# Performance work log

Hardware: AMD Instinct MI355X
Metric: run time of the kernel (lower is better)

The kernel has to match this reference:

```python
import jax, jax.numpy as jnp
import numpy as np

B, T, HID = 1, 2048, 2048
H = 16            # num_heads == num_key_value_heads
D = HID // H      # head_dim == feature_dim == 128
EPS = 1e-5


def _layer_norm(x, eps=1e-5):
    mu = jnp.mean(x, axis=-1, keepdims=True)
    var = jnp.mean((x - mu) ** 2, axis=-1, keepdims=True)
    return (x - mu) * jax.lax.rsqrt(var + eps)


def _feature_map(x, gamma, beta):
    # ReBased feature map, flatten=False (parallel mode): affine then LayerNorm
    return _layer_norm(x * gamma + beta)


def setup_inputs() -> dict:
    key = jax.random.key(0)
    ks = jax.random.split(key, 8)
    s = HID ** -0.5
    return {
        "hidden_states": jax.random.normal(ks[0], (B, T, HID), jnp.float32),
        "Wq": jax.random.normal(ks[1], (HID, HID), jnp.float32) * s,
        "Wk": jax.random.normal(ks[2], (HID, HID), jnp.float32) * s,
        "Wv": jax.random.normal(ks[3], (HID, HID), jnp.float32) * s,
        "Wo": jax.random.normal(ks[4], (HID, HID), jnp.float32) * s,
        "gamma": 1.0 + 0.1 * jax.random.normal(ks[5], (D,), jnp.float32),
        "beta": 0.1 * jax.random.normal(ks[6], (D,), jnp.float32),
    }


def reference(hidden_states, Wq, Wk, Wv, Wo, gamma, beta):
    b, t, _ = hidden_states.shape
    # projections (nn.Linear: x @ W.T), split into heads: [b, t, h, d]
    q = (hidden_states @ Wq.T).reshape(b, t, H, D)
    k = (hidden_states @ Wk.T).reshape(b, t, H, D)
    v = (hidden_states @ Wv.T).reshape(b, t, H, D)
    # ReBased feature map (no quadratic flatten in parallel mode)
    q = _feature_map(q, gamma, beta)
    k = _feature_map(k, gamma, beta)
    # parallel_rebased: scale q, quadratic score, causal mask, normalize
    q = q * (D ** -0.5)
    attn = jnp.einsum('bqhd,bkhd->bhqk', q, k) ** 2  # (q.k)^2
    mask = jnp.tril(jnp.ones((t, t), dtype=bool))
    attn = jnp.where(mask, attn, 0.0)
    o = jnp.einsum('bhqk,bkhd->bqhd', attn, v)       # [b, t, h, d]
    z = jnp.sum(attn, axis=-1)                       # [b, h, t]
    o = o / (jnp.swapaxes(z, 1, 2)[..., None] + EPS)
    o = o.reshape(b, t, H * D)
    return o @ Wo.T
```

## Files before the change

### kernel.cpp

```cpp
#include <hip/hip_runtime.h>
#include <hip/hip_bf16.h>
#include <stdint.h>

typedef __bf16 bf16;
typedef __bf16 v8bf __attribute__((ext_vector_type(8)));
typedef float  v4f  __attribute__((ext_vector_type(4)));

#define TSEQ   2048
#define HIDDIM 2048
#define NHEAD  16
#define HDIM   128

__device__ __forceinline__ void async16(void* lds, const void* g)
{
    __builtin_amdgcn_global_load_lds(
        (__attribute__((address_space(1))) void*)(uintptr_t)g,
        (__attribute__((address_space(3))) void*)(unsigned int)(uintptr_t)lds,
        16, 0, 0);
}

__global__ __launch_bounds__(256) void conv5(const float* __restrict__ s0, bf16* __restrict__ d0,
                                             const float* __restrict__ s1, bf16* __restrict__ d1,
                                             const float* __restrict__ s2, bf16* __restrict__ d2,
                                             const float* __restrict__ s3, bf16* __restrict__ d3,
                                             const float* __restrict__ s4, bf16* __restrict__ d4)
{
    const float* src; bf16* dst;
    switch (blockIdx.y) {
        case 0: src = s0; dst = d0; break;
        case 1: src = s1; dst = d1; break;
        case 2: src = s2; dst = d2; break;
        case 3: src = s3; dst = d3; break;
        default: src = s4; dst = d4; break;
    }
    const size_t i = ((size_t)blockIdx.x * 256 + threadIdx.x) * 8;
    const float4 a = *(const float4*)(src + i);
    const float4 b = *(const float4*)(src + i + 4);
    v8bf o;
    o[0] = (bf16)a.x; o[1] = (bf16)a.y; o[2] = (bf16)a.z; o[3] = (bf16)a.w;
    o[4] = (bf16)b.x; o[5] = (bf16)b.y; o[6] = (bf16)b.z; o[7] = (bf16)b.w;
    *(v8bf*)(dst + i) = o;
}

template <typename CT>
__device__ __forceinline__ void gemm_body(const bf16* __restrict__ A,
                                          const bf16* __restrict__ B,
                                          CT* __restrict__ C,
                                          int m0, int n0, int K, int ldc)
{
    __shared__ __attribute__((aligned(16))) bf16 sA[128*32];
    __shared__ __attribute__((aligned(16))) bf16 sB[128*32];
    const int tid  = threadIdx.x;
    const int lane = tid & 63;
    const int w    = tid >> 6;
    const int wm   = w >> 1, wn = w & 1;
    const int quad = lane >> 4, lr = lane & 15;
    const int srow = lane >> 2;
    const int scol = (lane & 3) * 8;

    const bf16* gA0 = A + (size_t)(m0 + w*32 + srow) * K + scol;
    const bf16* gB0 = B + (size_t)(n0 + w*32 + srow) * K + scol;
    bf16* lA0 = &sA[w*1024];
    bf16* lB0 = &sB[w*1024];

    v4f acc[4][4] = {};

    for (int kt = 0; kt < K; kt += 32) {
        __syncthreads();
        async16(lA0,       gA0 + kt);
        async16(lA0 + 512, gA0 + (size_t)16*K + kt);
        async16(lB0,       gB0 + kt);
        async16(lB0 + 512, gB0 + (size_t)16*K + kt);
        __syncthreads();
        v8bf a[4], b[4];
#pragma unroll
        for (int i = 0; i < 4; ++i)
            a[i] = *(const v8bf*)&sA[(wm*64 + i*16 + lr)*32 + quad*8];
#pragma unroll
        for (int j = 0; j < 4; ++j)
            b[j] = *(const v8bf*)&sB[(wn*64 + j*16 + lr)*32 + quad*8];
#pragma unroll
        for (int i = 0; i < 4; ++i)
#pragma unroll
            for (int j = 0; j < 4; ++j)
                acc[i][j] = __builtin_amdgcn_mfma_f32_16x16x32_bf16(a[i], b[j], acc[i][j], 0, 0, 0);
    }

#pragma unroll
    for (int i = 0; i < 4; ++i) {
        const int row_b = m0 + wm*64 + i*16 + quad*4;
#pragma unroll
        for (int j = 0; j < 4; ++j) {
            const int col = n0 + wn*64 + j*16 + lr;
#pragma unroll
            for (int r = 0; r < 4; ++r)
                C[(size_t)(row_b + r)*ldc + col] = (CT)acc[i][j][r];
        }
    }
}

__global__ __launch_bounds__(256) void gemm_qkv(const bf16* __restrict__ A,
    const bf16* __restrict__ Wq, const bf16* __restrict__ Wk, const bf16* __restrict__ Wv,
    bf16* __restrict__ qb, bf16* __restrict__ kb, bf16* __restrict__ vb)
{
    const int which = blockIdx.x >> 4;
    const int n0 = (blockIdx.x & 15) * 128;
    const int m0 = blockIdx.y * 128;
    const bf16* B = (which == 0) ? Wq : (which == 1) ? Wk : Wv;
    bf16* C = (which == 0) ? qb : (which == 1) ? kb : vb;
    gemm_body<bf16>(A, B, C, m0, n0, HIDDIM, HIDDIM);
}

__global__ __launch_bounds__(256) void gemm_out(const bf16* __restrict__ A,
    const bf16* __restrict__ B, float* __restrict__ C)
{
    __shared__ __attribute__((aligned(16))) bf16 sA[128*32];
    __shared__ __attribute__((aligned(16))) bf16 sB[64*32];
    const int m0 = blockIdx.y * 128, n0 = blockIdx.x * 64;
    const int K = HIDDIM, ldc = HIDDIM;
    const int tid  = threadIdx.x;
    const int lane = tid & 63;
    const int w    = tid >> 6;
    const int wm   = w >> 1, wn = w & 1;
    const int quad = lane >> 4, lr = lane & 15;
    const int srow = lane >> 2;
    const int scol = (lane & 3) * 8;

    const bf16* gA0 = A + (size_t)(m0 + w*32 + srow) * K + scol;
    const bf16* gB0 = B + (size_t)(n0 + w*16 + srow) * K + scol;
    bf16* lA0 = &sA[w*1024];
    bf16* lB0 = &sB[w*512];

    v4f acc[4][2] = {};

    for (int kt = 0; kt < K; kt += 32) {
        __syncthreads();
        async16(lA0,       gA0 + kt);
        async16(lA0 + 512, gA0 + (size_t)16*K + kt);
        async16(lB0,       gB0 + kt);
        __syncthreads();
        v8bf a[4], b[2];
#pragma unroll
        for (int i = 0; i < 4; ++i)
            a[i] = *(const v8bf*)&sA[(wm*64 + i*16 + lr)*32 + quad*8];
#pragma unroll
        for (int j = 0; j < 2; ++j)
            b[j] = *(const v8bf*)&sB[(wn*32 + j*16 + lr)*32 + quad*8];
#pragma unroll
        for (int i = 0; i < 4; ++i)
#pragma unroll
            for (int j = 0; j < 2; ++j)
                acc[i][j] = __builtin_amdgcn_mfma_f32_16x16x32_bf16(a[i], b[j], acc[i][j], 0, 0, 0);
    }

#pragma unroll
    for (int i = 0; i < 4; ++i) {
        const int row_b = m0 + wm*64 + i*16 + quad*4;
#pragma unroll
        for (int j = 0; j < 2; ++j) {
            const int col = n0 + wn*32 + j*16 + lr;
#pragma unroll
            for (int r = 0; r < 4; ++r)
                C[(size_t)(row_b + r)*ldc + col] = acc[i][j][r];
        }
    }
}

__global__ __launch_bounds__(256) void fmap(bf16* __restrict__ qb, bf16* __restrict__ kb,
                                            const float* __restrict__ gamma,
                                            const float* __restrict__ beta)
{
    const int rid  = blockIdx.x * 4 + (threadIdx.x >> 6);
    const int lane = threadIdx.x & 63;
    bf16* base = (rid < TSEQ*NHEAD) ? (qb + (size_t)rid * HDIM)
                                    : (kb + (size_t)(rid - TSEQ*NHEAD) * HDIM);
    const float scale = (rid < TSEQ*NHEAD) ? 0.08838834764831845f : 1.0f;

    const bf16 x0b = base[lane*2], x1b = base[lane*2+1];
    const float g0 = gamma[lane*2], g1 = gamma[lane*2+1];
    const float b0 = beta[lane*2],  b1 = beta[lane*2+1];
    float x0 = (float)x0b*g0 + b0;
    float x1 = (float)x1b*g1 + b1;
    float s  = x0 + x1;
    float sq = x0*x0 + x1*x1;
#pragma unroll
    for (int off = 1; off < 64; off <<= 1) { s += __shfl_xor(s, off); sq += __shfl_xor(sq, off); }
    const float mu   = s * (1.0f/128.0f);
    float var        = sq * (1.0f/128.0f) - mu*mu;
    var = fmaxf(var, 0.0f);
    const float rstd = rsqrtf(var + 1e-5f);
    base[lane*2]   = (bf16)((x0 - mu) * rstd * scale);
    base[lane*2+1] = (bf16)((x1 - mu) * rstd * scale);
}

__global__ __launch_bounds__(256) void transpose2048(const bf16* __restrict__ src,
                                                     bf16* __restrict__ dst)
{
    __shared__ __attribute__((aligned(16))) bf16 tile[64][72];
    const int t0 = blockIdx.y * 64, c0 = blockIdx.x * 64;
    const int tid = threadIdx.x;
    const int r = tid >> 3;
    const int c = (tid & 7) * 8;
#pragma unroll
    for (int p = 0; p < 2; ++p) {
        const int rr = r + p*32;
        *(v8bf*)&tile[rr][c] = *(const v8bf*)(src + (size_t)(t0+rr)*HIDDIM + c0 + c);
    }
    __syncthreads();
#pragma unroll
    for (int p = 0; p < 2; ++p) {
        const int orow = r + p*32;
        v8bf o;
#pragma unroll
        for (int i = 0; i < 8; ++i) o[i] = tile[c + i][orow];
        *(v8bf*)(dst + (size_t)(c0+orow)*HIDDIM + t0 + c) = o;
    }
}

__global__ __launch_bounds__(256) void attn(const bf16* __restrict__ qb,
                                            const bf16* __restrict__ kb,
                                            const bf16* __restrict__ vt,
                                            bf16* __restrict__ ob)
{
    __shared__ __attribute__((aligned(16))) bf16 sK[64*136];
    __shared__ __attribute__((aligned(16))) bf16 sV[128*72];
    __shared__ __attribute__((aligned(16))) bf16 sS[64*72];
    const int h    = blockIdx.y;
    const int tile = 31 - blockIdx.x;
    const int tid  = threadIdx.x, lane = tid & 63, w = tid >> 6;
    const int quad = lane >> 4, lr = lane & 15;

    v8bf qa[4];
    {
        const bf16* q0 = qb + (size_t)(tile*64 + w*16 + lr)*HIDDIM + h*HDIM + quad*8;
#pragma unroll
        for (int ks = 0; ks < 4; ++ks)
            qa[ks] = *(const v8bf*)(q0 + ks*32);
    }

    const int rK = tid >> 4, cK = (tid & 15) * 8;
    const int rV = tid >> 3, cV = (tid & 7) * 8;

    v8bf curK[4], curV[4], nxtK[4], nxtV[4];
#pragma unroll
    for (int p = 0; p < 4; ++p) {
        curK[p] = *(const v8bf*)(kb + (size_t)(rK + p*16)*HIDDIM + h*HDIM + cK);
        curV[p] = *(const v8bf*)(vt + (size_t)(h*HDIM + rV + p*32)*HIDDIM + cV);
    }

    v4f  o[8] = {};
    float z[4] = {};
    const int nch = tile + 1;

    for (int ch = 0; ch < nch; ++ch) {
        const int s0 = ch * 64;
        const bool diag = (ch == tile);
        __syncthreads();
#pragma unroll
        for (int p = 0; p < 4; ++p)
            *(v8bf*)&sK[(rK + p*16)*136 + cK] = curK[p];
#pragma unroll
        for (int p = 0; p < 4; ++p)
            *(v8bf*)&sV[(rV + p*32)*72 + cV] = curV[p];
        if (ch + 1 < nch) {
            const int s1 = s0 + 64;
#pragma unroll
            for (int p = 0; p < 4; ++p) {
                nxtK[p] = *(const v8bf*)(kb + (size_t)(s1 + rK + p*16)*HIDDIM + h*HDIM + cK);
                nxtV[p] = *(const v8bf*)(vt + (size_t)(h*HDIM + rV + p*32)*HIDDIM + s1 + cV);
            }
        }
        __syncthreads();

        v8bf kbf[4][4];
#pragma unroll
        for (int nj = 0; nj < 4; ++nj)
#pragma unroll
            for (int ks = 0; ks < 4; ++ks)
                kbf[nj][ks] = *(const v8bf*)&sK[(nj*16 + lr)*136 + ks*32 + quad*8];
        const int row_l = w*16 + quad*4;
        const int qg    = tile*64 + row_l;
#pragma unroll
        for (int nj = 0; nj < 4; ++nj) {
            v4f s4 = {0.f, 0.f, 0.f, 0.f};
#pragma unroll
            for (int ks = 0; ks < 4; ++ks)
                s4 = __builtin_amdgcn_mfma_f32_16x16x32_bf16(qa[ks], kbf[nj][ks], s4, 0, 0, 0);
            const int col = nj*16 + lr;
            const int sg  = s0 + col;
#pragma unroll
            for (int r = 0; r < 4; ++r) {
                float val = s4[r] * s4[r];
                if (diag && (sg > qg + r)) val = 0.0f;
                const bf16 vb16 = (bf16)val;
                z[r] += (float)vb16;
                sS[(row_l + r)*72 + col] = vb16;
            }
        }

#pragma unroll
        for (int ks = 0; ks < 2; ++ks) {
            const v8bf sa = *(const v8bf*)&sS[(w*16 + lr)*72 + ks*32 + quad*8];
#pragma unroll
            for (int nd = 0; nd < 8; ++nd) {
                const v8bf vbf = *(const v8bf*)&sV[(nd*16 + lr)*72 + ks*32 + quad*8];
                o[nd] = __builtin_amdgcn_mfma_f32_16x16x32_bf16(sa, vbf, o[nd], 0, 0, 0);
            }
        }

        if (ch + 1 < nch) {
#pragma unroll
            for (int p = 0; p < 4; ++p) { curK[p] = nxtK[p]; curV[p] = nxtV[p]; }
        }
    }

#pragma unroll
    for (int r = 0; r < 4; ++r) {
        float zz = z[r];
        zz += __shfl_xor(zz, 1); zz += __shfl_xor(zz, 2);
        zz += __shfl_xor(zz, 4); zz += __shfl_xor(zz, 8);
        z[r] = zz + 1e-5f;
    }

    {
        const int row_l = w*16 + quad*4;
        const size_t rbase = (size_t)(tile*64 + row_l)*HIDDIM + h*HDIM;
#pragma unroll
        for (int nd = 0; nd < 8; ++nd) {
            const int col = nd*16 + lr;
#pragma unroll
            for (int r = 0; r < 4; ++r)
                ob[rbase + (size_t)r*HIDDIM + col] = (bf16)(o[nd][r] / z[r]);
        }
    }
}

extern "C" void kernel_launch(void* const* d_in, const int* in_sizes, int n_in,
                              void* d_out, int out_size, void* d_ws, size_t ws_size,
                              hipStream_t stream)
{
    const float* hs    = (const float*)d_in[0];
    const float* Wq    = (const float*)d_in[1];
    const float* Wk    = (const float*)d_in[2];
    const float* Wv    = (const float*)d_in[3];
    const float* Wo    = (const float*)d_in[4];
    const float* gamma = (const float*)d_in[5];
    const float* beta  = (const float*)d_in[6];
    float* outp = (float*)d_out;

    const size_t MAT = (size_t)TSEQ * HIDDIM;

    bf16* ws   = (bf16*)d_ws;
    bf16* hs_b = ws + 0*MAT;
    bf16* vt   = hs_b;
    bf16* Wv_b = ws + 1*MAT;
    bf16* Wo_b = ws + 2*MAT;
    bf16* qb   = ws + 3*MAT;
    bf16* kb   = ws + 4*MAT;
    bf16* vb   = ws + 5*MAT;
    bf16* ob   = vb;
    bf16* Wq_b = (bf16*)d_out;
    bf16* Wk_b = (bf16*)d_out + MAT;

    conv5<<<dim3(2048, 5), 256, 0, stream>>>(hs, hs_b, Wq, Wq_b, Wk, Wk_b, Wv, Wv_b, Wo, Wo_b);
    gemm_qkv<<<dim3(48, 16), 256, 0, stream>>>(hs_b, Wq_b, Wk_b, Wv_b, qb, kb, vb);
    fmap<<<dim3(2*TSEQ*NHEAD/4), 256, 0, stream>>>(qb, kb, gamma, beta);
    transpose2048<<<dim3(32, 32), 256, 0, stream>>>(vb, vt);
    attn<<<dim3(32, 16), 256, 0, stream>>>(qb, kb, vt, ob);
    gemm_out<<<dim3(32, 16), 256, 0, stream>>>(ob, Wo_b, outp);
}
```

Measured before the change: 301.4 us.

## Fuse feature-map LayerNorm and V transpose into QKV GEMM epilogue

```diff
diff --git a/kernel.cpp b/kernel.cpp
--- a/kernel.cpp
+++ b/kernel.cpp
@@ -42,14 +42,21 @@
     *(v8bf*)(dst + i) = o;
 }
 
-template <typename CT>
-__device__ __forceinline__ void gemm_body(const bf16* __restrict__ A,
-                                          const bf16* __restrict__ B,
-                                          CT* __restrict__ C,
-                                          int m0, int n0, int K, int ldc)
+__global__ __launch_bounds__(256) void gemm_qkv(const bf16* __restrict__ A,
+    const bf16* __restrict__ Wq, const bf16* __restrict__ Wk, const bf16* __restrict__ Wv,
+    const float* __restrict__ gamma, const float* __restrict__ beta,
+    bf16* __restrict__ qb, bf16* __restrict__ kb, bf16* __restrict__ vt)
 {
     __shared__ __attribute__((aligned(16))) bf16 sA[128*32];
     __shared__ __attribute__((aligned(16))) bf16 sB[128*32];
+    __shared__ __attribute__((aligned(16))) bf16 sEpi[128*136];
+
+    const int which = blockIdx.x >> 4;
+    const int n0 = (blockIdx.x & 15) * 128;
+    const int m0 = blockIdx.y * 128;
+    const bf16* B = (which == 0) ? Wq : (which == 1) ? Wk : Wv;
+    const int K = HIDDIM;
+
     const int tid  = threadIdx.x;
     const int lane = tid & 63;
     const int w    = tid >> 6;
@@ -86,29 +93,83 @@
                 acc[i][j] = __builtin_amdgcn_mfma_f32_16x16x32_bf16(a[i], b[j], acc[i][j], 0, 0, 0);
     }
 
-#pragma unroll
-    for (int i = 0; i < 4; ++i) {
-        const int row_b = m0 + wm*64 + i*16 + quad*4;
+    if (which < 2) {
+        bf16* C = (which == 0) ? qb : kb;
+        const float scale = (which == 0) ? 0.08838834764831845f : 1.0f;
+        float g[4], bt[4];
 #pragma unroll
         for (int j = 0; j < 4; ++j) {
-            const int col = n0 + wn*64 + j*16 + lr;
-#pragma unroll
-            for (int r = 0; r < 4; ++r)
-                C[(size_t)(row_b + r)*ldc + col] = (CT)acc[i][j][r];
-        }
-    }
-}
-
-__global__ __launch_bounds__(256) void gemm_qkv(const bf16* __restrict__ A,
-    const bf16* __restrict__ Wq, const bf16* __restrict__ Wk, const bf16* __restrict__ Wv,
-    bf16* __restrict__ qb, bf16* __restrict__ kb, bf16* __restrict__ vb)
-{
-    const int which = blockIdx.x >> 4;
-    const int n0 = (blockIdx.x & 15) * 128;
-    const int m0 = blockIdx.y * 128;
-    const bf16* B = (which == 0) ? Wq : (which == 1) ? Wk : Wv;
-    bf16* C = (which == 0) ? qb : (which == 1) ? kb : vb;
-    gemm_body<bf16>(A, B, C, m0, n0, HIDDIM, HIDDIM);
+            const int col_l = wn*64 + j*16 + lr;
+            g[j]  = gamma[col_l];
+            bt[j] = beta[col_l];
+        }
+#pragma unroll
+        for (int i = 0; i < 4; ++i)
+#pragma unroll
+            for (int j = 0; j < 4; ++j)
+#pragma unroll
+                for (int r = 0; r < 4; ++r)
+                    acc[i][j][r] = acc[i][j][r]*g[j] + bt[j];
+
+        float* part = (float*)sEpi;
+#pragma unroll
+        for (int i = 0; i < 4; ++i)
+#pragma unroll
+            for (int r = 0; r < 4; ++r) {
+                float s = 0.f, q = 0.f;
+#pragma unroll
+                for (int j = 0; j < 4; ++j) { s += acc[i][j][r]; q += acc[i][j][r]*acc[i][j][r]; }
+                s += __shfl_xor(s, 1); q += __shfl_xor(q, 1);
+                s += __shfl_xor(s, 2); q += __shfl_xor(q, 2);
+                s += __shfl_xor(s, 4); q += __shfl_xor(q, 4);
+                s += __shfl_xor(s, 8); q += __shfl_xor(q, 8);
+                if (lr == 0) {
+                    const int row_l = wm*64 + i*16 + quad*4 + r;
+                    part[row_l*4 + wn*2 + 0] = s;
+                    part[row_l*4 + wn*2 + 1] = q;
+                }
+            }
+        __syncthreads();
+#pragma unroll
+        for (int i = 0; i < 4; ++i)
+#pragma unroll
+            for (int r = 0; r < 4; ++r) {
+                const int row_l = wm*64 + i*16 + quad*4 + r;
+                const float s  = part[row_l*4 + 0] + part[row_l*4 + 2];
+                const float q  = part[row_l*4 + 1] + part[row_l*4 + 3];
+                const float mu = s * (1.0f/128.0f);
+                float var = q * (1.0f/128.0f) - mu*mu;
+                var = fmaxf(var, 0.0f);
+                const float rstd = rsqrtf(var + 1e-5f) * scale;
+#pragma unroll
+                for (int j = 0; j < 4; ++j) {
+                    const int col = n0 + wn*64 + j*16 + lr;
+                    C[(size_t)(m0 + row_l)*HIDDIM + col] = (bf16)((acc[i][j][r] - mu) * rstd);
+                }
+            }
+    } else {
+#pragma unroll
+        for (int i = 0; i < 4; ++i)
+#pragma unroll
+            for (int j = 0; j < 4; ++j) {
+                const int row_l = wm*64 + i*16 + quad*4;
+                const int col_l = wn*64 + j*16 + lr;
+#pragma unroll
+                for (int r = 0; r < 4; ++r)
+                    sEpi[(row_l + r)*136 + col_l] = (bf16)acc[i][j][r];
+            }
+        __syncthreads();
+        const int c  = tid >> 1;
+        const int rh = tid & 1;
+#pragma unroll
+        for (int k = 0; k < 8; ++k) {
+            v8bf o;
+#pragma unroll
+            for (int i = 0; i < 8; ++i)
+                o[i] = sEpi[(rh*64 + k*8 + i)*136 + c];
+            *(v8bf*)(vt + (size_t)(n0 + c)*HIDDIM + m0 + rh*64 + k*8) = o;
+        }
+    }
 }
 
 __global__ __launch_bounds__(256) void gemm_out(const bf16* __restrict__ A,
@@ -166,57 +227,6 @@
     }
 }
 
-__global__ __launch_bounds__(256) void fmap(bf16* __restrict__ qb, bf16* __restrict__ kb,
-                                            const float* __restrict__ gamma,
-                                            const float* __restrict__ beta)
-{
-    const int rid  = blockIdx.x * 4 + (threadIdx.x >> 6);
-    const int lane = threadIdx.x & 63;
-    bf16* base = (rid < TSEQ*NHEAD) ? (qb + (size_t)rid * HDIM)
-                                    : (kb + (size_t)(rid - TSEQ*NHEAD) * HDIM);
-    const float scale = (rid < TSEQ*NHEAD) ? 0.08838834764831845f : 1.0f;
-
-    const bf16 x0b = base[lane*2], x1b = base[lane*2+1];
-    const float g0 = gamma[lane*2], g1 = gamma[lane*2+1];
-    const float b0 = beta[lane*2],  b1 = beta[lane*2+1];
-    float x0 = (float)x0b*g0 + b0;
-    float x1 = (float)x1b*g1 + b1;
-    float s  = x0 + x1;
-    float sq = x0*x0 + x1*x1;
-#pragma unroll
-    for (int off = 1; off < 64; off <<= 1) { s += __shfl_xor(s, off); sq += __shfl_xor(sq, off); }
-    const float mu   = s * (1.0f/128.0f);
-    float var        = sq * (1.0f/128.0f) - mu*mu;
-    var = fmaxf(var, 0.0f);
-    const float rstd = rsqrtf(var + 1e-5f);
-    base[lane*2]   = (bf16)((x0 - mu) * rstd * scale);
-    base[lane*2+1] = (bf16)((x1 - mu) * rstd * scale);
-}
-
-__global__ __launch_bounds__(256) void transpose2048(const bf16* __restrict__ src,
-                                                     bf16* __restrict__ dst)
-{
-    __shared__ __attribute__((aligned(16))) bf16 tile[64][72];
-    const int t0 = blockIdx.y * 64, c0 = blockIdx.x * 64;
-    const int tid = threadIdx.x;
-    const int r = tid >> 3;
-    const int c = (tid & 7) * 8;
-#pragma unroll
-    for (int p = 0; p < 2; ++p) {
-        const int rr = r + p*32;
-        *(v8bf*)&tile[rr][c] = *(const v8bf*)(src + (size_t)(t0+rr)*HIDDIM + c0 + c);
-    }
-    __syncthreads();
-#pragma unroll
-    for (int p = 0; p < 2; ++p) {
-        const int orow = r + p*32;
-        v8bf o;
-#pragma unroll
-        for (int i = 0; i < 8; ++i) o[i] = tile[c + i][orow];
-        *(v8bf*)(dst + (size_t)(c0+orow)*HIDDIM + t0 + c) = o;
-    }
-}
-
 __global__ __launch_bounds__(256) void attn(const bf16* __restrict__ qb,
                                             const bf16* __restrict__ kb,
                                             const bf16* __restrict__ vt,
@@ -352,20 +362,17 @@
 
     bf16* ws   = (bf16*)d_ws;
     bf16* hs_b = ws + 0*MAT;
-    bf16* vt   = hs_b;
     bf16* Wv_b = ws + 1*MAT;
     bf16* Wo_b = ws + 2*MAT;
     bf16* qb   = ws + 3*MAT;
     bf16* kb   = ws + 4*MAT;
-    bf16* vb   = ws + 5*MAT;
-    bf16* ob   = vb;
+    bf16* vt   = ws + 5*MAT;
+    bf16* ob   = hs_b;
     bf16* Wq_b = (bf16*)d_out;
     bf16* Wk_b = (bf16*)d_out + MAT;
 
     conv5<<<dim3(2048, 5), 256, 0, stream>>>(hs, hs_b, Wq, Wq_b, Wk, Wk_b, Wv, Wv_b, Wo, Wo_b);
-    gemm_qkv<<<dim3(48, 16), 256, 0, stream>>>(hs_b, Wq_b, Wk_b, Wv_b, qb, kb, vb);
-    fmap<<<dim3(2*TSEQ*NHEAD/4), 256, 0, stream>>>(qb, kb, gamma, beta);
-    transpose2048<<<dim3(32, 32), 256, 0, stream>>>(vb, vt);
+    gemm_qkv<<<dim3(48, 16), 256, 0, stream>>>(hs_b, Wq_b, Wk_b, Wv_b, gamma, beta, qb, kb, vt);
     attn<<<dim3(32, 16), 256, 0, stream>>>(qb, kb, vt, ob);
     gemm_out<<<dim3(32, 16), 256, 0, stream>>>(ob, Wo_b, outp);
 }
```

Result: slower. 315.8 us (+4.8%).
